# Optimization experiments

Measured on AMD Instinct MI355X. Metric: run time of the kernel, lower is better.

Reference implementation:

```python
import jax, jax.numpy as jnp
import numpy as np

N = 10000      # nodes
E = 160000     # directed edges
D_IN = 256     # node input feature dim
D_EIN = 128    # edge input feature dim
D = 256        # pretrans / hidden dim


def setup_inputs() -> dict:
    key = jax.random.key(0)
    ks = jax.random.split(key, 10)

    def w(k, shape):
        fan_in = shape[0]
        return jax.random.normal(k, shape, jnp.float32) * (1.0 / np.sqrt(fan_in))

    return {
        "x": jax.random.normal(ks[0], (N, D_IN), jnp.float32),
        "edge_feat": jax.random.normal(ks[1], (E, D_EIN), jnp.float32),
        "edge_index": jax.random.randint(ks[2], (2, E), 0, N),  # row0=src, row1=dst
        "Wn": w(ks[3], (D_IN, D)), "bn": jnp.zeros((D,), jnp.float32),
        "We": w(ks[4], (D_EIN, D)), "be": jnp.zeros((D,), jnp.float32),
        "Wpa": w(ks[5], (2 * D, D)), "bpa": jnp.zeros((D,), jnp.float32),
        "Wsa": w(ks[6], (2 * D, D)), "bsa": jnp.zeros((D,), jnp.float32),
        "Wnt": w(ks[7], (3 * D, D)), "bnt": jnp.zeros((D,), jnp.float32),
        "Wet": w(ks[8], (3 * D, D)), "bet": jnp.zeros((D,), jnp.float32),
    }


def reference(x, edge_feat, edge_index, Wn, bn, We, be, Wpa, bpa, Wsa, bsa, Wnt, bnt, Wet, bet):
    src, dst = edge_index[0], edge_index[1]

    # pretrans stage (per-node / per-edge MLPs)
    pre_n = jax.nn.relu(x @ Wn + bn)           # [N, D]
    pre_e = jax.nn.relu(edge_feat @ We + be)   # [E, D]

    ones = jnp.ones((pre_e.shape[0],), pre_n.dtype)
    deg_in = jax.ops.segment_sum(ones, dst, num_segments=N)   # predecessors per node
    deg_out = jax.ops.segment_sum(ones, src, num_segments=N)  # successors per node

    # predecessor aggregation at v: edges u->v, message = MLP(cat(pre_n[u], pre_e))
    msg_p = jax.nn.relu(jnp.concatenate([pre_n[src], pre_e], axis=-1) @ Wpa + bpa)  # [E, D]
    agg_p = jax.ops.segment_sum(msg_p, dst, num_segments=N) / jnp.maximum(deg_in, 1.0)[:, None]

    # successor aggregation at u: edges u->v, message = MLP(cat(pre_n[v], pre_e))
    msg_s = jax.nn.relu(jnp.concatenate([pre_n[dst], pre_e], axis=-1) @ Wsa + bsa)  # [E, D]
    agg_s = jax.ops.segment_sum(msg_s, src, num_segments=N) / jnp.maximum(deg_out, 1.0)[:, None]

    # node transformer on stack([pred_agg, self_pretrans, succ_agg]) -> flatten
    node_out = jnp.concatenate([agg_p, pre_n, agg_s], axis=-1) @ Wnt + bnt  # [N, D]

    # edge transformer on stack([src_pretrans, edge_pretrans, dst_pretrans])
    edge_out = jnp.concatenate([pre_n[src], pre_e, pre_n[dst]], axis=-1) @ Wet + bet  # [E, D]

    return node_out, edge_out
```

## Files before the change

### kernel.cpp

```cpp
#include <hip/hip_runtime.h>
#include <hip/hip_bf16.h>

#define N_NODES 10000
#define N_EDGES 160000
#define DD      256

typedef __bf16 bf16x8 __attribute__((ext_vector_type(8)));
typedef float  f32x4  __attribute__((ext_vector_type(4)));

__global__ void prep_weights_kernel(
    const float* __restrict__ Wn, const float* __restrict__ We,
    const float* __restrict__ Wnt, const float* __restrict__ Wpa,
    const float* __restrict__ Wsa, const float* __restrict__ Wet,
    __hip_bfloat16* __restrict__ Wn_t, __hip_bfloat16* __restrict__ We_t,
    __hip_bfloat16* __restrict__ Wnt_t, __hip_bfloat16* __restrict__ We_edge,
    __hip_bfloat16* __restrict__ Wn_node) {
  int idx = blockIdx.x * 256 + threadIdx.x;
  if (idx < 65536) {
    const int n = idx >> 8, k = idx & 255;
    Wn_t[idx] = __float2bfloat16(Wn[k * 256 + n]);
    return;
  }
  idx -= 65536;
  if (idx < 32768) {
    const int n = idx >> 7, k = idx & 127;
    We_t[idx] = __float2bfloat16(We[k * 256 + n]);
    return;
  }
  idx -= 32768;
  if (idx < 196608) {
    const int n = idx / 768, k = idx % 768;
    Wnt_t[idx] = __float2bfloat16(Wnt[k * 256 + n]);
    return;
  }
  idx -= 196608;
  if (idx < 196608) {
    const int n = idx >> 8, k = idx & 255;
    float v;
    if (n < 256)      v = Wpa[(256 + k) * 256 + n];
    else if (n < 512) v = Wsa[(256 + k) * 256 + (n - 256)];
    else              v = Wet[(256 + k) * 256 + (n - 512)];
    We_edge[idx] = __float2bfloat16(v);
    return;
  }
  idx -= 196608;
  if (idx < 262144) {
    const int n = idx >> 8, k = idx & 255;
    float v;
    if (n < 256)      v = Wpa[k * 256 + n];
    else if (n < 512) v = Wsa[k * 256 + (n - 256)];
    else if (n < 768) v = Wet[k * 256 + (n - 512)];
    else              v = Wet[(512 + k) * 256 + (n - 768)];
    Wn_node[idx] = __float2bfloat16(v);
  }
}

__global__ void count_kernel(const int* __restrict__ src, const int* __restrict__ dst,
                             int* __restrict__ cnt_out, int* __restrict__ cnt_in) {
  const int e = blockIdx.x * 256 + threadIdx.x;
  if (e < N_EDGES) {
    atomicAdd(&cnt_out[src[e]], 1);
    atomicAdd(&cnt_in[dst[e]], 1);
  }
}

__global__ __launch_bounds__(256) void scan2_kernel(
    const int* __restrict__ cnt_in, const int* __restrict__ cnt_out,
    int* __restrict__ offs_in, int* __restrict__ offs_out) {
  const int* cnt = blockIdx.x ? cnt_out : cnt_in;
  int* offs      = blockIdx.x ? offs_out : offs_in;
  const int n = N_NODES;
  __shared__ int part[256];
  const int t  = threadIdx.x;
  const int lo = t * 40;
  const int hi = (lo + 40 < n) ? lo + 40 : n;
  int s = 0;
  for (int i = lo; i < hi; ++i) s += cnt[i];
  part[t] = s;
  __syncthreads();
  for (int off = 1; off < 256; off <<= 1) {
    int v = (t >= off) ? part[t - off] : 0;
    __syncthreads();
    part[t] += v;
    __syncthreads();
  }
  int run = (t == 0) ? 0 : part[t - 1];
  for (int i = lo; i < hi; ++i) { offs[i] = run; run += cnt[i]; }
  if (t == 255) offs[n] = run;
}

__global__ void fill_kernel(const int* __restrict__ src, const int* __restrict__ dst,
                            const int* __restrict__ offs_out, const int* __restrict__ offs_in,
                            int* __restrict__ cur_out, int* __restrict__ cur_in,
                            int* __restrict__ pos_out, int* __restrict__ pos_in) {
  const int e = blockIdx.x * 256 + threadIdx.x;
  if (e < N_EDGES) {
    const int u = src[e];
    pos_out[e] = offs_out[u] + atomicAdd(&cur_out[u], 1);
    const int v = dst[e];
    pos_in[e] = offs_in[v] + atomicAdd(&cur_in[v], 1);
  }
}

template <bool RELU, bool F32OUT, bool A_F32>
__global__ __launch_bounds__(512, 4) void gemm_mfma_kernel(
    const void* __restrict__ Av, const __hip_bfloat16* __restrict__ Wt,
    const float* __restrict__ bias, float* __restrict__ outf,
    __hip_bfloat16* __restrict__ outb, int M, int Ksteps, int ldo) {
  __shared__ char sA[2][16384];
  __shared__ char sW[2][16384];

  const int K    = Ksteps * 64;
  const int row0 = blockIdx.x * 128;
  const int nt   = blockIdx.y;

  const int tid  = threadIdx.x;
  const int lane = tid & 63;
  const int w    = tid >> 6;

  const int rsub  = lane >> 3;
  const int pslot = lane & 7;
  const int sslot = pslot ^ rsub;

  auto stage = [&](int b, int c) {
#pragma unroll
    for (int j = 0; j < 2; ++j) {
      const int r = w * 16 + j * 8 + rsub;
      int ar = row0 + r;
      if (ar >= M) ar = M - 1;
      if constexpr (A_F32) {
        const float* gp = (const float*)Av + (size_t)ar * K + c * 64 + sslot * 8;
        const f32x4 lo = *(const f32x4*)gp;
        const f32x4 hi = *(const f32x4*)(gp + 4);
        union { __hip_bfloat16 h[8]; bf16x8 v; } pk;
#pragma unroll
        for (int q = 0; q < 4; ++q) pk.h[q] = __float2bfloat16(lo[q]);
#pragma unroll
        for (int q = 0; q < 4; ++q) pk.h[4 + q] = __float2bfloat16(hi[q]);
        *(bf16x8*)&sA[b][r * 128 + pslot * 16] = pk.v;
      } else {
        const __hip_bfloat16* gp =
            (const __hip_bfloat16*)Av + (size_t)ar * K + c * 64 + sslot * 8;
        __builtin_amdgcn_global_load_lds(
            (const __attribute__((address_space(1))) void*)gp,
            (__attribute__((address_space(3))) void*)&sA[b][(w * 16 + j * 8) * 128],
            16, 0, 0);
      }
      const __hip_bfloat16* wp = Wt + (size_t)(nt * 128 + r) * K + c * 64 + sslot * 8;
      __builtin_amdgcn_global_load_lds(
          (const __attribute__((address_space(1))) void*)wp,
          (__attribute__((address_space(3))) void*)&sW[b][(w * 16 + j * 8) * 128],
          16, 0, 0);
    }
  };

  const int wm = (w >> 1) * 32;
  const int wn = (w & 1) * 64;

  f32x4 acc[2][4];
#pragma unroll
  for (int i = 0; i < 2; ++i)
#pragma unroll
    for (int j = 0; j < 4; ++j) acc[i][j] = (f32x4)0.f;

  stage(0, 0);
  asm volatile("s_waitcnt vmcnt(0)");
  __syncthreads();

  int buf = 0;
  for (int c = 0; c < Ksteps; ++c) {
    if (c + 1 < Ksteps) stage(buf ^ 1, c + 1);
#pragma unroll
    for (int kk = 0; kk < 2; ++kk) {
      bf16x8 av[2], bv[4];
#pragma unroll
      for (int i = 0; i < 2; ++i) {
        const int row  = wm + i * 16 + (lane & 15);
        const int boff = row * 128 + ((kk * 64 + (lane >> 4) * 16) ^ ((row & 7) << 4));
        av[i] = *(const bf16x8*)&sA[buf][boff];
      }
#pragma unroll
      for (int j = 0; j < 4; ++j) {
        const int nrow = wn + j * 16 + (lane & 15);
        const int boff = nrow * 128 + ((kk * 64 + (lane >> 4) * 16) ^ ((nrow & 7) << 4));
        bv[j] = *(const bf16x8*)&sW[buf][boff];
      }
#pragma unroll
      for (int i = 0; i < 2; ++i)
#pragma unroll
        for (int j = 0; j < 4; ++j)
          acc[i][j] = __builtin_amdgcn_mfma_f32_16x16x32_bf16(av[i], bv[j], acc[i][j], 0, 0, 0);
    }
    __syncthreads();
    buf ^= 1;
  }

#pragma unroll
  for (int i = 0; i < 2; ++i) {
    const int row = row0 + wm + i * 16 + ((lane >> 4) << 2);
#pragma unroll
    for (int j = 0; j < 4; ++j) {
      const int col = nt * 128 + wn + j * 16 + (lane & 15);
      const float bb = bias ? bias[col] : 0.f;
#pragma unroll
      for (int r = 0; r < 4; ++r) {
        if (row + r < M) {
          float v = acc[i][j][r] + bb;
          if (RELU) v = v > 0.f ? v : 0.f;
          if (F32OUT) outf[(size_t)(row + r) * ldo + col] = v;
          else        outb[(size_t)(row + r) * ldo + col] = __float2bfloat16(v);
        }
      }
    }
  }
}

template <bool MSG>
__global__ __launch_bounds__(512, 4) void edge_mfma_kernel(
    const float* __restrict__ ef,
    const __hip_bfloat16* __restrict__ We_t,
    const float* __restrict__ be,
    const __hip_bfloat16* __restrict__ We,
    const __hip_bfloat16* __restrict__ nodeP,
    const int* __restrict__ src, const int* __restrict__ dst,
    const int* __restrict__ pos_in, const int* __restrict__ pos_out,
    const float* __restrict__ bpa, const float* __restrict__ bsa,
    const float* __restrict__ bet,
    float* __restrict__ agg_p, float* __restrict__ agg_s,
    __hip_bfloat16* __restrict__ msg_p, __hip_bfloat16* __restrict__ msg_s,
    float* __restrict__ edge_out) {
  __shared__ char sA[4][8192];
  __shared__ char sW[2][16384];
  __shared__ int sSrc[64], sDst[64], sPin[64], sPout[64];

  const int et = blockIdx.x;
  const int e0 = et * 64;

  const int tid  = threadIdx.x;
  const int lane = tid & 63;
  const int w    = tid >> 6;

  if (tid < 64)        sSrc[tid] = src[e0 + tid];
  else if (tid < 128)  sDst[tid - 64] = dst[e0 + tid - 64];
  else if (tid < 192) { if (MSG) sPin[tid - 128]  = pos_in[e0 + tid - 128]; }
  else if (tid < 256) { if (MSG) sPout[tid - 192] = pos_out[e0 + tid - 192]; }

  const int rsub  = lane >> 3;
  const int pslot = lane & 7;
  const int sslot = pslot ^ rsub;

  const int wm = (w >> 1) * 16;
  const int wn = (w & 1) * 64;

  {
    const int r  = tid >> 3;
    const int s0 = tid & 7;
#pragma unroll
    for (int t = 0; t < 2; ++t) {
      const int s  = s0 + t * 8;
      const int kb = s >> 3;
      const int ss = s & 7;
      const float* gp = ef + (size_t)(e0 + r) * 128 + s * 8;
      const f32x4 lo = *(const f32x4*)gp;
      const f32x4 hi = *(const f32x4*)(gp + 4);
      union { __hip_bfloat16 h[8]; bf16x8 v; } pk;
#pragma unroll
      for (int q = 0; q < 4; ++q) pk.h[q] = __float2bfloat16(lo[q]);
#pragma unroll
      for (int q = 0; q < 4; ++q) pk.h[4 + q] = __float2bfloat16(hi[q]);
      *(bf16x8*)&sA[kb][r * 128 + ((ss * 16) ^ ((r & 7) << 4))] = pk.v;
    }
  }

  auto stageWt = [&](int h) {
#pragma unroll
    for (int j = 0; j < 2; ++j) {
      const int r = w * 16 + j * 8 + rsub;
#pragma unroll
      for (int kb = 0; kb < 2; ++kb) {
        const __hip_bfloat16* gp =
            We_t + (size_t)(h * 128 + r) * 128 + kb * 64 + sslot * 8;
        __builtin_amdgcn_global_load_lds(
            (const __attribute__((address_space(1))) void*)gp,
            (__attribute__((address_space(3))) void*)&sW[kb][(w * 16 + j * 8) * 128],
            16, 0, 0);
      }
    }
  };

  auto stageW = [&](int b, int t) {
    const int nt = t >> 2, c = t & 3;
#pragma unroll
    for (int j = 0; j < 2; ++j) {
      const int r = w * 16 + j * 8 + rsub;
      const __hip_bfloat16* wp = We + (size_t)(nt * 128 + r) * 256 + c * 64 + sslot * 8;
      __builtin_amdgcn_global_load_lds(
          (const __attribute__((address_space(1))) void*)wp,
          (__attribute__((address_space(3))) void*)&sW[b][(w * 16 + j * 8) * 128],
          16, 0, 0);
    }
  };

  f32x4 accA0[4], accA1[4];
#pragma unroll
  for (int j = 0; j < 4; ++j) { accA0[j] = (f32x4)0.f; accA1[j] = (f32x4)0.f; }

  stageWt(0);
  asm volatile("s_waitcnt vmcnt(0)");
  __syncthreads();

#pragma unroll
  for (int kb = 0; kb < 2; ++kb) {
#pragma unroll
    for (int kk = 0; kk < 2; ++kk) {
      const int row  = wm + (lane & 15);
      const int aoff = row * 128 + ((kk * 64 + (lane >> 4) * 16) ^ ((row & 7) << 4));
      const bf16x8 av = *(const bf16x8*)&sA[kb][aoff];
#pragma unroll
      for (int j = 0; j < 4; ++j) {
        const int nrow = wn + j * 16 + (lane & 15);
        const int boff = nrow * 128 + ((kk * 64 + (lane >> 4) * 16) ^ ((nrow & 7) << 4));
        const bf16x8 bv = *(const bf16x8*)&sW[kb][boff];
        accA0[j] = __builtin_amdgcn_mfma_f32_16x16x32_bf16(av, bv, accA0[j], 0, 0, 0);
      }
    }
  }
  __syncthreads();
  stageWt(1);
  asm volatile("s_waitcnt vmcnt(0)");
  __syncthreads();
#pragma unroll
  for (int kb = 0; kb < 2; ++kb) {
#pragma unroll
    for (int kk = 0; kk < 2; ++kk) {
      const int row  = wm + (lane & 15);
      const int aoff = row * 128 + ((kk * 64 + (lane >> 4) * 16) ^ ((row & 7) << 4));
      const bf16x8 av = *(const bf16x8*)&sA[kb][aoff];
#pragma unroll
      for (int j = 0; j < 4; ++j) {
        const int nrow = wn + j * 16 + (lane & 15);
        const int boff = nrow * 128 + ((kk * 64 + (lane >> 4) * 16) ^ ((nrow & 7) << 4));
        const bf16x8 bv = *(const bf16x8*)&sW[kb][boff];
        accA1[j] = __builtin_amdgcn_mfma_f32_16x16x32_bf16(av, bv, accA1[j], 0, 0, 0);
      }
    }
  }
  __syncthreads();

  stageW(0, 0);

  {
    const int rowb = wm + ((lane >> 4) << 2);
#pragma unroll
    for (int h = 0; h < 2; ++h) {
#pragma unroll
      for (int j = 0; j < 4; ++j) {
        const int col  = h * 128 + wn + j * 16 + (lane & 15);
        const float bb = be[col];
        const int c    = col >> 6;
        const int cb2  = (col & 63) * 2;
#pragma unroll
        for (int r = 0; r < 4; ++r) {
          const int row = rowb + r;
          float v = (h == 0 ? accA0[j][r] : accA1[j][r]) + bb;
          v = v > 0.f ? v : 0.f;
          *(__hip_bfloat16*)&sA[c][row * 128 + (cb2 ^ ((row & 7) << 4))] =
              __float2bfloat16(v);
        }
      }
    }
  }

  asm volatile("s_waitcnt vmcnt(0)");
  __syncthreads();

  int buf = 0;
  for (int nt = 0; nt < 6; ++nt) {
    const int mat = nt >> 1;
    f32x4 acc[4];
#pragma unroll
    for (int j = 0; j < 4; ++j) acc[j] = (f32x4)0.f;

#pragma unroll
    for (int c = 0; c < 4; ++c) {
      const int t = nt * 4 + c;
      if (t + 1 < 24) stageW(buf ^ 1, t + 1);
#pragma unroll
      for (int kk = 0; kk < 2; ++kk) {
        const int row  = wm + (lane & 15);
        const int aoff = row * 128 + ((kk * 64 + (lane >> 4) * 16) ^ ((row & 7) << 4));
        const bf16x8 av = *(const bf16x8*)&sA[c][aoff];
        bf16x8 bv[4];
#pragma unroll
        for (int j = 0; j < 4; ++j) {
          const int nrow = wn + j * 16 + (lane & 15);
          const int boff = nrow * 128 + ((kk * 64 + (lane >> 4) * 16) ^ ((nrow & 7) << 4));
          bv[j] = *(const bf16x8*)&sW[buf][boff];
        }
#pragma unroll
        for (int j = 0; j < 4; ++j)
          acc[j] = __builtin_amdgcn_mfma_f32_16x16x32_bf16(av, bv[j], acc[j], 0, 0, 0);
      }
      __syncthreads();
      buf ^= 1;
    }

    const int colbase = (nt & 1) * 128 + wn;
    const int lrow = wm + ((lane >> 4) << 2);
#pragma unroll
    for (int j = 0; j < 4; ++j) {
      const int col = colbase + j * 16 + (lane & 15);
      if (mat == 0) {
        const float bb = bpa[col];
#pragma unroll
        for (int r = 0; r < 4; ++r) {
          const int le = lrow + r;
          float v = acc[j][r] + bb +
                    __bfloat162float(nodeP[(size_t)sSrc[le] * 1024 + col]);
          v = v > 0.f ? v : 0.f;
          if (MSG) msg_p[(size_t)sPin[le] * 256 + col] = __float2bfloat16(v);
          else     atomicAdd(&agg_p[(size_t)sDst[le] * 256 + col], v);
        }
      } else if (mat == 1) {
        const float bb = bsa[col];
#pragma unroll
        for (int r = 0; r < 4; ++r) {
          const int le = lrow + r;
          float v = acc[j][r] + bb +
                    __bfloat162float(nodeP[(size_t)sDst[le] * 1024 + 256 + col]);
          v = v > 0.f ? v : 0.f;
          if (MSG) msg_s[(size_t)sPout[le] * 256 + col] = __float2bfloat16(v);
          else     atomicAdd(&agg_s[(size_t)sSrc[le] * 256 + col], v);
        }
      } else {
        const float bb = bet[col];
#pragma unroll
        for (int r = 0; r < 4; ++r) {
          const int le = lrow + r;
          float v = acc[j][r] + bb +
                    __bfloat162float(nodeP[(size_t)sSrc[le] * 1024 + 512 + col]) +
                    __bfloat162float(nodeP[(size_t)sDst[le] * 1024 + 768 + col]);
          edge_out[(size_t)(e0 + le) * 256 + col] = v;
        }
      }
    }
  }
}

__global__ __launch_bounds__(256) void agg_kernel(
    const __hip_bfloat16* __restrict__ msg_p, const __hip_bfloat16* __restrict__ msg_s,
    const __hip_bfloat16* __restrict__ pre_n,
    const int* __restrict__ offs_in, const int* __restrict__ offs_out,
    __hip_bfloat16* __restrict__ nodeH) {
  __shared__ float part[2][32][8];

  const int v    = blockIdx.x;
  const int tid  = threadIdx.x;
  const int dir  = tid >> 7;
  const int sub  = tid & 127;
  const int wsub = sub >> 6;
  const int lane = sub & 63;
  const int cg   = lane & 31;
  const int par  = wsub * 2 + (lane >> 5);

  const int* offs = dir ? offs_out : offs_in;
  const __hip_bfloat16* msg = dir ? msg_s : msg_p;

  const int p0 = offs[v], p1 = offs[v + 1];
  float acc[8];
#pragma unroll
  for (int k = 0; k < 8; ++k) acc[k] = 0.f;

  for (int i = p0 + par; i < p1; i += 4) {
    const uint4 u = *(const uint4*)(msg + (size_t)i * 256 + cg * 8);
    const unsigned short* h = (const unsigned short*)&u;
#pragma unroll
    for (int k = 0; k < 8; ++k) acc[k] += __uint_as_float((unsigned)h[k] << 16);
  }
#pragma unroll
  for (int k = 0; k < 8; ++k) acc[k] += __shfl_xor(acc[k], 32);

  if (wsub == 1 && (lane >> 5) == 0) {
#pragma unroll
    for (int k = 0; k < 8; ++k) part[dir][cg][k] = acc[k];
  }
  __syncthreads();

  if (wsub == 0 && (lane >> 5) == 0) {
    const int deg = p1 - p0;
    const float inv = 1.f / (float)(deg > 1 ? deg : 1);
    union { __hip_bfloat16 h[8]; uint4 u; } o;
#pragma unroll
    for (int k = 0; k < 8; ++k)
      o.h[k] = __float2bfloat16((acc[k] + part[dir][cg][k]) * inv);
    *(uint4*)(nodeH + (size_t)v * 768 + dir * 512 + cg * 8) = o.u;
  } else if (wsub == 0 && dir == 0) {
    const uint4 u = *(const uint4*)(pre_n + (size_t)v * 256 + cg * 8);
    *(uint4*)(nodeH + (size_t)v * 768 + 256 + cg * 8) = u;
  }
}

__global__ void node_prep_kernel(const float* __restrict__ agg_p,
                                 const float* __restrict__ agg_s,
                                 const __hip_bfloat16* __restrict__ pre_n,
                                 const int* __restrict__ cnt_in,
                                 const int* __restrict__ cnt_out,
                                 __hip_bfloat16* __restrict__ nodeH) {
  const int row = blockIdx.x;
  const int c   = threadIdx.x;
  const float di = (float)(cnt_in[row]  > 1 ? cnt_in[row]  : 1);
  const float dd = (float)(cnt_out[row] > 1 ? cnt_out[row] : 1);
  nodeH[(size_t)row * 768 + c]       = __float2bfloat16(agg_p[(size_t)row * 256 + c] / di);
  nodeH[(size_t)row * 768 + 256 + c] = pre_n[(size_t)row * 256 + c];
  nodeH[(size_t)row * 768 + 512 + c] = __float2bfloat16(agg_s[(size_t)row * 256 + c] / dd);
}

extern "C" void kernel_launch(void* const* d_in, const int* in_sizes, int n_in,
                              void* d_out, int out_size, void* d_ws, size_t ws_size,
                              hipStream_t stream) {
  const float* x         = (const float*)d_in[0];
  const float* edge_feat = (const float*)d_in[1];
  const int*   edge_idx  = (const int*)d_in[2];
  const float* Wn  = (const float*)d_in[3];
  const float* bn  = (const float*)d_in[4];
  const float* We  = (const float*)d_in[5];
  const float* be  = (const float*)d_in[6];
  const float* Wpa = (const float*)d_in[7];
  const float* bpa = (const float*)d_in[8];
  const float* Wsa = (const float*)d_in[9];
  const float* bsa = (const float*)d_in[10];
  const float* Wnt = (const float*)d_in[11];
  const float* bnt = (const float*)d_in[12];
  const float* Wet = (const float*)d_in[13];
  const float* bet = (const float*)d_in[14];

  const int* src = edge_idx;
  const int* dst = edge_idx + N_EDGES;

  float* node_out = (float*)d_out;
  float* edge_out = (float*)d_out + (size_t)N_NODES * DD;

  char* p = (char*)d_ws;
  auto alloc = [&](size_t bytes) -> void* {
    void* r = (void*)p;
    p += (bytes + 255) & ~(size_t)255;
    return r;
  };

  __hip_bfloat16* pre_n_bf = (__hip_bfloat16*)alloc((size_t)N_NODES * DD * 2);
  __hip_bfloat16* nodeH    = (__hip_bfloat16*)alloc((size_t)N_NODES * 768 * 2);
  __hip_bfloat16* nodeP    = (__hip_bfloat16*)alloc((size_t)N_NODES * 1024 * 2);
  __hip_bfloat16* We_edge  = (__hip_bfloat16*)alloc((size_t)768 * 256 * 2);
  __hip_bfloat16* Wn_node  = (__hip_bfloat16*)alloc((size_t)1024 * 256 * 2);
  __hip_bfloat16* Wn_t     = (__hip_bfloat16*)alloc((size_t)256 * 256 * 2);
  __hip_bfloat16* We_t     = (__hip_bfloat16*)alloc((size_t)256 * 128 * 2);
  __hip_bfloat16* Wnt_t    = (__hip_bfloat16*)alloc((size_t)256 * 768 * 2);
  int* csr_zero = (int*)alloc(4 * (size_t)N_NODES * 4);
  int* cnt_in   = csr_zero;
  int* cnt_out  = csr_zero + N_NODES;
  int* cur_in   = csr_zero + 2 * N_NODES;
  int* cur_out  = csr_zero + 3 * N_NODES;
  int* offs_in  = (int*)alloc(((size_t)N_NODES + 1) * 4);
  int* offs_out = (int*)alloc(((size_t)N_NODES + 1) * 4);
  int* pos_in   = (int*)alloc((size_t)N_EDGES * 4);
  int* pos_out  = (int*)alloc((size_t)N_EDGES * 4);

  const size_t msg_bytes = (size_t)N_EDGES * DD * 2;
  const size_t base_used = (size_t)(p - (char*)d_ws);
  const bool msg_mode = ws_size >= base_used + 2 * msg_bytes + 512;

  __hip_bfloat16* msg_p = nullptr;
  __hip_bfloat16* msg_s = nullptr;
  float* agg_p = nullptr;
  float* agg_s = nullptr;
  if (msg_mode) {
    msg_p = (__hip_bfloat16*)alloc(msg_bytes);
    msg_s = (__hip_bfloat16*)alloc(msg_bytes);
  } else {
    agg_p = (float*)alloc((size_t)N_NODES * DD * 4);
    agg_s = (float*)alloc((size_t)N_NODES * DD * 4);
  }

  hipMemsetAsync(csr_zero, 0, 4 * (size_t)N_NODES * 4, stream);
  if (!msg_mode)
    hipMemsetAsync(agg_p, 0, 2 * (size_t)N_NODES * DD * 4, stream);

  prep_weights_kernel<<<(753664 + 255) / 256, 256, 0, stream>>>(
      Wn, We, Wnt, Wpa, Wsa, Wet, Wn_t, We_t, Wnt_t, We_edge, Wn_node);

  count_kernel<<<(N_EDGES + 255) / 256, 256, 0, stream>>>(src, dst, cnt_out, cnt_in);
  if (msg_mode) {
    scan2_kernel<<<2, 256, 0, stream>>>(cnt_in, cnt_out, offs_in, offs_out);
    fill_kernel<<<(N_EDGES + 255) / 256, 256, 0, stream>>>(
        src, dst, offs_out, offs_in, cur_out, cur_in, pos_out, pos_in);
  }

  {
    dim3 g((N_NODES + 127) / 128, 2);
    gemm_mfma_kernel<true, false, true><<<g, 512, 0, stream>>>(
        x, Wn_t, bn, nullptr, pre_n_bf, N_NODES, 4, 256);
  }
  {
    dim3 g((N_NODES + 127) / 128, 8);
    gemm_mfma_kernel<false, false, false><<<g, 512, 0, stream>>>(
        pre_n_bf, Wn_node, nullptr, nullptr, nodeP, N_NODES, 4, 1024);
  }

  if (msg_mode) {
    edge_mfma_kernel<true><<<N_EDGES / 64, 512, 0, stream>>>(
        edge_feat, We_t, be, We_edge, nodeP, src, dst, pos_in, pos_out,
        bpa, bsa, bet, nullptr, nullptr, msg_p, msg_s, edge_out);
    agg_kernel<<<N_NODES, 256, 0, stream>>>(
        msg_p, msg_s, pre_n_bf, offs_in, offs_out, nodeH);
  } else {
    edge_mfma_kernel<false><<<N_EDGES / 64, 512, 0, stream>>>(
        edge_feat, We_t, be, We_edge, nodeP, src, dst, nullptr, nullptr,
        bpa, bsa, bet, agg_p, agg_s, nullptr, nullptr, edge_out);
    node_prep_kernel<<<N_NODES, 256, 0, stream>>>(
        agg_p, agg_s, pre_n_bf, cnt_in, cnt_out, nodeH);
  }

  {
    dim3 g((N_NODES + 127) / 128, 2);
    gemm_mfma_kernel<false, true, false><<<g, 512, 0, stream>>>(
        nodeH, Wnt_t, bnt, node_out, nullptr, N_NODES, 12, 256);
  }
}
```

Before: 343.2 us.

## Triple-buffer weight staging and read edge indices directly from global

The weight-tile pipeline in the edge MFMA kernel moves from a double buffer to a triple buffer with a two-tile prefetch distance. The per-chunk __syncthreads is replaced by an explicit vmcnt wait plus s_barrier so loads can stay in flight across iterations. The shared-memory copies of src/dst/pos indices are dropped, and each epilogue loads them as int4 vectors from global memory. The extra 16 KB of LDS per block may lower occupancy below the launch-bounds target, and the vmcnt counts depend on how many loads stageW issues.

```diff
diff --git a/kernel.cpp b/kernel.cpp
--- a/kernel.cpp
+++ b/kernel.cpp
@@ -230,8 +230,7 @@
     __hip_bfloat16* __restrict__ msg_p, __hip_bfloat16* __restrict__ msg_s,
     float* __restrict__ edge_out) {
   __shared__ char sA[4][8192];
-  __shared__ char sW[2][16384];
-  __shared__ int sSrc[64], sDst[64], sPin[64], sPout[64];
+  __shared__ char sW[3][16384];
 
   const int et = blockIdx.x;
   const int e0 = et * 64;
@@ -239,11 +238,6 @@
   const int tid  = threadIdx.x;
   const int lane = tid & 63;
   const int w    = tid >> 6;
-
-  if (tid < 64)        sSrc[tid] = src[e0 + tid];
-  else if (tid < 128)  sDst[tid - 64] = dst[e0 + tid - 64];
-  else if (tid < 192) { if (MSG) sPin[tid - 128]  = pos_in[e0 + tid - 128]; }
-  else if (tid < 256) { if (MSG) sPout[tid - 192] = pos_out[e0 + tid - 192]; }
 
   const int rsub  = lane >> 3;
   const int pslot = lane & 7;
@@ -347,8 +341,6 @@
   }
   __syncthreads();
 
-  stageW(0, 0);
-
   {
     const int rowb = wm + ((lane >> 4) << 2);
 #pragma unroll
@@ -371,10 +363,14 @@
     }
   }
 
-  asm volatile("s_waitcnt vmcnt(0)");
-  __syncthreads();
-
-  int buf = 0;
+  stageW(0, 0);
+  stageW(1, 1);
+  asm volatile("s_waitcnt vmcnt(2) lgkmcnt(0)" ::: "memory");
+  __builtin_amdgcn_sched_barrier(0);
+  __builtin_amdgcn_s_barrier();
+  __builtin_amdgcn_sched_barrier(0);
+
+  int cur = 0;
   for (int nt = 0; nt < 6; ++nt) {
     const int mat = nt >> 1;
     f32x4 acc[4];
@@ -384,7 +380,9 @@
 #pragma unroll
     for (int c = 0; c < 4; ++c) {
       const int t = nt * 4 + c;
-      if (t + 1 < 24) stageW(buf ^ 1, t + 1);
+      int nxt2 = cur + 2; if (nxt2 >= 3) nxt2 -= 3;
+      const bool more = (t + 2 < 24);
+      if (more) stageW(nxt2, t + 2);
 #pragma unroll
       for (int kk = 0; kk < 2; ++kk) {
         const int row  = wm + (lane & 15);
@@ -395,14 +393,19 @@
         for (int j = 0; j < 4; ++j) {
           const int nrow = wn + j * 16 + (lane & 15);
           const int boff = nrow * 128 + ((kk * 64 + (lane >> 4) * 16) ^ ((nrow & 7) << 4));
-          bv[j] = *(const bf16x8*)&sW[buf][boff];
+          bv[j] = *(const bf16x8*)&sW[cur][boff];
         }
 #pragma unroll
         for (int j = 0; j < 4; ++j)
           acc[j] = __builtin_amdgcn_mfma_f32_16x16x32_bf16(av, bv[j], acc[j], 0, 0, 0);
       }
-      __syncthreads();
-      buf ^= 1;
+      __builtin_amdgcn_sched_barrier(0);
+      if (more) asm volatile("s_waitcnt vmcnt(2)" ::: "memory");
+      else      asm volatile("s_waitcnt vmcnt(0)" ::: "memory");
+      __builtin_amdgcn_sched_barrier(0);
+      __builtin_amdgcn_s_barrier();
+      __builtin_amdgcn_sched_barrier(0);
+      cur = cur + 1; if (cur >= 3) cur = 0;
     }
 
     const int colbase = (nt & 1) * 128 + wn;
@@ -411,36 +414,69 @@
     for (int j = 0; j < 4; ++j) {
       const int col = colbase + j * 16 + (lane & 15);
       if (mat == 0) {
+        const int4 gat = *(const int4*)(src + e0 + lrow);
         const float bb = bpa[col];
-#pragma unroll
-        for (int r = 0; r < 4; ++r) {
-          const int le = lrow + r;
-          float v = acc[j][r] + bb +
-                    __bfloat162float(nodeP[(size_t)sSrc[le] * 1024 + col]);
-          v = v > 0.f ? v : 0.f;
-          if (MSG) msg_p[(size_t)sPin[le] * 256 + col] = __float2bfloat16(v);
-          else     atomicAdd(&agg_p[(size_t)sDst[le] * 256 + col], v);
+        if (MSG) {
+          const int4 ps = *(const int4*)(pos_in + e0 + lrow);
+          const int pv[4] = {ps.x, ps.y, ps.z, ps.w};
+          const int gv[4] = {gat.x, gat.y, gat.z, gat.w};
+#pragma unroll
+          for (int r = 0; r < 4; ++r) {
+            float v = acc[j][r] + bb +
+                      __bfloat162float(nodeP[(size_t)gv[r] * 1024 + col]);
+            v = v > 0.f ? v : 0.f;
+            msg_p[(size_t)pv[r] * 256 + col] = __float2bfloat16(v);
+          }
+        } else {
+          const int4 dd = *(const int4*)(dst + e0 + lrow);
+          const int gv[4] = {gat.x, gat.y, gat.z, gat.w};
+          const int dv[4] = {dd.x, dd.y, dd.z, dd.w};
+#pragma unroll
+          for (int r = 0; r < 4; ++r) {
+            float v = acc[j][r] + bb +
+                      __bfloat162float(nodeP[(size_t)gv[r] * 1024 + col]);
+            v = v > 0.f ? v : 0.f;
+            atomicAdd(&agg_p[(size_t)dv[r] * 256 + col], v);
+          }
         }
       } else if (mat == 1) {
+        const int4 gat = *(const int4*)(dst + e0 + lrow);
         const float bb = bsa[col];
-#pragma unroll
-        for (int r = 0; r < 4; ++r) {
-          const int le = lrow + r;
-          float v = acc[j][r] + bb +
-                    __bfloat162float(nodeP[(size_t)sDst[le] * 1024 + 256 + col]);
-          v = v > 0.f ? v : 0.f;
-          if (MSG) msg_s[(size_t)sPout[le] * 256 + col] = __float2bfloat16(v);
-          else     atomicAdd(&agg_s[(size_t)sSrc[le] * 256 + col], v);
+        if (MSG) {
+          const int4 ps = *(const int4*)(pos_out + e0 + lrow);
+          const int pv[4] = {ps.x, ps.y, ps.z, ps.w};
+          const int gv[4] = {gat.x, gat.y, gat.z, gat.w};
+#pragma unroll
+          for (int r = 0; r < 4; ++r) {
+            float v = acc[j][r] + bb +
+                      __bfloat162float(nodeP[(size_t)gv[r] * 1024 + 256 + col]);
+            v = v > 0.f ? v : 0.f;
+            msg_s[(size_t)pv[r] * 256 + col] = __float2bfloat16(v);
+          }
+        } else {
+          const int4 ss = *(const int4*)(src + e0 + lrow);
+          const int gv[4] = {gat.x, gat.y, gat.z, gat.w};
+          const int sv[4] = {ss.x, ss.y, ss.z, ss.w};
+#pragma unroll
+          for (int r = 0; r < 4; ++r) {
+            float v = acc[j][r] + bb +
+                      __bfloat162float(nodeP[(size_t)gv[r] * 1024 + 256 + col]);
+            v = v > 0.f ? v : 0.f;
+            atomicAdd(&agg_s[(size_t)sv[r] * 256 + col], v);
+          }
         }
       } else {
+        const int4 ss = *(const int4*)(src + e0 + lrow);
+        const int4 dd = *(const int4*)(dst + e0 + lrow);
+        const int sv[4] = {ss.x, ss.y, ss.z, ss.w};
+        const int dv[4] = {dd.x, dd.y, dd.z, dd.w};
         const float bb = bet[col];
 #pragma unroll
         for (int r = 0; r < 4; ++r) {
-          const int le = lrow + r;
           float v = acc[j][r] + bb +
-                    __bfloat162float(nodeP[(size_t)sSrc[le] * 1024 + 512 + col]) +
-                    __bfloat162float(nodeP[(size_t)sDst[le] * 1024 + 768 + col]);
-          edge_out[(size_t)(e0 + le) * 256 + col] = v;
+                    __bfloat162float(nodeP[(size_t)sv[r] * 1024 + 512 + col]) +
+                    __bfloat162float(nodeP[(size_t)dv[r] * 1024 + 768 + col]);
+          edge_out[(size_t)(e0 + lrow + r) * 256 + col] = v;
         }
       }
     }
```

Measured after the change: 364.1 us. 1.06x slower.
